# Kernel tuning notes

Hardware: AMD Instinct MI355X
Metric: run time of the kernel (lower is better)

The kernel has to match this reference:

```python
import jax, jax.numpy as jnp
import numpy as np

B, C, H, W = 512, 128, 7, 7
P = 21            # patch_size
DIL = 2           # dilation_patch
PAD = DIL * (P // 2)  # 20: max displacement in pixels


def setup_inputs() -> dict:
    key = jax.random.key(0)
    k1, k2, k3, k4 = jax.random.split(key, 4)
    patch1 = jax.random.normal(k1, (B, C, H, W), jnp.float32)
    patch2 = jax.random.normal(k2, (B, C, H, W), jnp.float32)
    feat = P * P * H * W  # 21609
    w_bbox = jax.random.normal(k3, (4, feat), jnp.float32) * (1.0 / np.sqrt(feat))
    b_bbox = jax.random.normal(k4, (4,), jnp.float32) * 0.01
    return {"patch1": patch1, "patch2": patch2, "w_bbox": w_bbox, "b_bbox": b_bbox}


def _correlation(patch1, patch2):
    """SpatialCorrelationSampler(patch_size=21, dilation_patch=2, kernel_size=1).

    out[b,p,q,i,j] = sum_c patch1[b,c,i,j] * patch2[b,c, i + 2*(p-10), j + 2*(q-10)]
    with zero padding for out-of-bounds displacements. Output: [B, 21, 21, 7, 7].
    """
    padded = jnp.pad(patch2, ((0, 0), (0, 0), (PAD, PAD), (PAD, PAD)))  # [B,C,47,47]
    # Outer product over spatial positions, contracted over channels:
    # T[b,i,j,u,v] = sum_c patch1[b,c,i,j] * padded[b,c,u,v]
    T = jnp.einsum('bcij,bcuv->bijuv', patch1, padded)  # [B,7,7,47,47]
    # Gather the displaced entries: u = 2p + i, v = 2q + j
    Pp, Qq, Ii, Jj = jnp.meshgrid(jnp.arange(P), jnp.arange(P),
                                  jnp.arange(H), jnp.arange(W), indexing='ij')
    corr = T[:, Ii, Jj, DIL * Pp + Ii, DIL * Qq + Jj]  # [B,21,21,7,7]
    return corr


def reference(patch1, patch2, w_bbox, b_bbox):
    corr = _correlation(patch1, patch2)           # [B,21,21,7,7]
    x = corr.reshape(corr.shape[0], -1)           # flatten(start_dim=1)
    return x @ w_bbox.T + b_bbox                  # [B,4]
```

## Files before the change

kernel.cpp:

```cpp
#include <hip/hip_runtime.h>

#define NB    512
#define FEAT  21609
#define CHW   6272
#define NV4   1568
#define PLANE 5120

__device__ __forceinline__ unsigned short f2bf(float x) {
    unsigned u = __float_as_uint(x);
    u += 0x7fffu + ((u >> 16) & 1u);
    return (unsigned short)(u >> 16);
}
__device__ __forceinline__ float bf2f(unsigned short h) {
    return __uint_as_float((unsigned)h << 16);
}

__global__ __launch_bounds__(256) void corr_head_kernel(
    const float* __restrict__ patch1,
    const float* __restrict__ patch2,
    const float* __restrict__ w_bbox,
    const float* __restrict__ b_bbox,
    float* __restrict__ out)
{
    __shared__ __align__(16) unsigned short s1b[CHW];
    __shared__ __align__(16) float          s2p[2 * PLANE];
    __shared__ __align__(16) ushort4        s_wq[784];
    __shared__ float s_red[16];

    const int tid = threadIdx.x;
    const int b   = blockIdx.x;

    for (int n = tid; n < 1024; n += 256) {
        int jp = n >> 9, c = (n >> 2) & 127, u = n & 3;
        s2p[jp * PLANE + c * 40 + 28 + u] = 0.f;
    }
    for (int n = tid; n < 896; n += 256) {
        int c = n / 7, i2 = n - 7 * c;
        s2p[PLANE + c * 40 + i2 * 4 + 3] = 0.f;
    }

    const float4* g1 = (const float4*)(patch1 + (size_t)b * CHW);
    for (int t = tid; t < NV4; t += 256) {
        float4 v = g1[t];
        ((ushort4*)s1b)[t] = make_ushort4(f2bf(v.x), f2bf(v.y), f2bf(v.z), f2bf(v.w));
    }

    const float4* g2 = (const float4*)(patch2 + (size_t)b * CHW);
    for (int t = tid; t < NV4; t += 256) {
        float4 v = g2[t];
        int e = t * 4;
        int c = e / 49;
        int r = e - 49 * c;
        #pragma unroll
        for (int k = 0; k < 4; ++k) {
            int i2 = (r * 37) >> 8;
            int j2 = r - 7 * i2;
            s2p[(j2 & 1) * PLANE + c * 40 + i2 * 4 + (j2 >> 1)] = (&v.x)[k];
            if (++r == 49) { r = 0; ++c; }
        }
    }

    for (int n = tid; n < 784; n += 256) {
        int ij = n % 49, tu = n / 49;
        int t = tu >> 2, u = tu & 3;
        int i = ij / 7, j = ij - 7 * i;
        int i2 = (i & 1) + 2 * t, j2 = (j & 1) + 2 * u;
        ushort4 wq = make_ushort4(0, 0, 0, 0);
        if (i2 < 7 && j2 < 7) {
            int p = 10 + ((i2 - i) >> 1);
            int q = 10 + ((j2 - j) >> 1);
            int f = ((p * 21 + q) * 7 + i) * 7 + j;
            wq = make_ushort4(f2bf(w_bbox[f]), f2bf(w_bbox[FEAT + f]),
                              f2bf(w_bbox[2 * FEAT + f]), f2bf(w_bbox[3 * FEAT + f]));
        }
        s_wq[n] = wq;
    }
    __syncthreads();

    float a0 = 0.f, a1 = 0.f, a2 = 0.f, a3 = 0.f;
    if (tid < 196) {
        const int ij = tid >> 2, cs = tid & 3;
        const int i = ij / 7, j = ij - 7 * i;
        const float* base2 = s2p + (j & 1) * PLANE + (i & 1) * 4;

        float dot[4][4];
        #pragma unroll
        for (int t = 0; t < 4; ++t)
            #pragma unroll
            for (int u = 0; u < 4; ++u) dot[t][u] = 0.f;

        #pragma unroll 2
        for (int cc = 0; cc < 32; ++cc) {
            int c = cs + 4 * cc;
            float f1 = bf2f(s1b[c * 49 + ij]);
            const float* bc = base2 + c * 40;
            #pragma unroll
            for (int t = 0; t < 4; ++t) {
                float4 f2 = *(const float4*)(bc + 8 * t);
                dot[t][0] = fmaf(f1, f2.x, dot[t][0]);
                dot[t][1] = fmaf(f1, f2.y, dot[t][1]);
                dot[t][2] = fmaf(f1, f2.z, dot[t][2]);
                dot[t][3] = fmaf(f1, f2.w, dot[t][3]);
            }
        }

        #pragma unroll
        for (int t = 0; t < 4; ++t)
            #pragma unroll
            for (int u = 0; u < 4; ++u) {
                ushort4 wq = s_wq[(4 * t + u) * 49 + ij];
                float d = dot[t][u];
                a0 = fmaf(d, bf2f(wq.x), a0);
                a1 = fmaf(d, bf2f(wq.y), a1);
                a2 = fmaf(d, bf2f(wq.z), a2);
                a3 = fmaf(d, bf2f(wq.w), a3);
            }
    }

    for (int off = 32; off > 0; off >>= 1) {
        a0 += __shfl_down(a0, off, 64);
        a1 += __shfl_down(a1, off, 64);
        a2 += __shfl_down(a2, off, 64);
        a3 += __shfl_down(a3, off, 64);
    }
    if ((tid & 63) == 0) {
        int w = tid >> 6;
        s_red[w * 4 + 0] = a0;
        s_red[w * 4 + 1] = a1;
        s_red[w * 4 + 2] = a2;
        s_red[w * 4 + 3] = a3;
    }
    __syncthreads();
    if (tid < 4) {
        float r = s_red[tid] + s_red[4 + tid] + s_red[8 + tid] + s_red[12 + tid];
        out[b * 4 + tid] = r + b_bbox[tid];
    }
}

extern "C" void kernel_launch(void* const* d_in, const int* in_sizes, int n_in,
                              void* d_out, int out_size, void* d_ws, size_t ws_size,
                              hipStream_t stream) {
    const float* patch1 = (const float*)d_in[0];
    const float* patch2 = (const float*)d_in[1];
    const float* w_bbox = (const float*)d_in[2];
    const float* b_bbox = (const float*)d_in[3];
    float* out = (float*)d_out;
    corr_head_kernel<<<dim3(NB), dim3(256), 0, stream>>>(patch1, patch2, w_bbox, b_bbox, out);
}
```

Baseline: 80.65 us.

## Prefetch all inputs into registers and overlap second half staging with compute

All global loads for patch1, patch2 and the weight gather are now issued up front into registers. The first half of the channels is written to shared memory and computed on while the second half and the weights are being staged. This is meant to hide global-load latency behind the first half's FMA work within each block. In exchange it uses more registers, which may lower occupancy, and adds an extra barrier.

```diff
diff --git a/kernel.cpp b/kernel.cpp
--- a/kernel.cpp
+++ b/kernel.cpp
@@ -3,8 +3,9 @@
 #define NB    512
 #define FEAT  21609
 #define CHW   6272
-#define NV4   1568
 #define PLANE 5120
+#define HV4   784
+#define HFLT  3136
 
 __device__ __forceinline__ unsigned short f2bf(float x) {
     unsigned u = __float_as_uint(x);
@@ -40,57 +41,75 @@
     }
 
     const float4* g1 = (const float4*)(patch1 + (size_t)b * CHW);
-    for (int t = tid; t < NV4; t += 256) {
-        float4 v = g1[t];
-        ((ushort4*)s1b)[t] = make_ushort4(f2bf(v.x), f2bf(v.y), f2bf(v.z), f2bf(v.w));
-    }
-
     const float4* g2 = (const float4*)(patch2 + (size_t)b * CHW);
-    for (int t = tid; t < NV4; t += 256) {
-        float4 v = g2[t];
-        int e = t * 4;
-        int c = e / 49;
-        int r = e - 49 * c;
+    float4 rp1[4], rp2[4], rq1[4], rq2[4];
+    #pragma unroll
+    for (int i = 0; i < 3; ++i) {
+        rp1[i] = g1[tid + 256 * i];
+        rp2[i] = g2[tid + 256 * i];
+        rq1[i] = g1[HV4 + tid + 256 * i];
+        rq2[i] = g2[HV4 + tid + 256 * i];
+    }
+    if (tid < 16) {
+        rp1[3] = g1[768 + tid];        rp2[3] = g2[768 + tid];
+        rq1[3] = g1[HV4 + 768 + tid];  rq2[3] = g2[HV4 + 768 + tid];
+    }
+
+    float wv[4][4];
+    #pragma unroll
+    for (int i = 0; i < 4; ++i) {
+        int n = tid + 256 * i;
+        wv[i][0] = wv[i][1] = wv[i][2] = wv[i][3] = 0.f;
+        if (n < 784) {
+            int ij = n % 49, tu = n / 49;
+            int t = tu >> 2, u = tu & 3;
+            int ii = ij / 7, jj = ij - 7 * ii;
+            int i2 = (ii & 1) + 2 * t, j2 = (jj & 1) + 2 * u;
+            if (i2 < 7 && j2 < 7) {
+                int p = 10 + ((i2 - ii) >> 1);
+                int q = 10 + ((j2 - jj) >> 1);
+                int f = ((p * 21 + q) * 7 + ii) * 7 + jj;
+                wv[i][0] = w_bbox[f];
+                wv[i][1] = w_bbox[FEAT + f];
+                wv[i][2] = w_bbox[2 * FEAT + f];
+                wv[i][3] = w_bbox[3 * FEAT + f];
+            }
+        }
+    }
+
+    #pragma unroll
+    for (int i = 0; i < 4; ++i) {
+        if (i < 3 || tid < 16) {
+            int t = tid + 256 * i;
+            float4 v = rp1[i];
+            ((ushort4*)s1b)[t] = make_ushort4(f2bf(v.x), f2bf(v.y), f2bf(v.z), f2bf(v.w));
+            float4 w = rp2[i];
+            int e = 4 * t;
+            int c = e / 49, r = e - 49 * c;
+            #pragma unroll
+            for (int k = 0; k < 4; ++k) {
+                int i2 = (r * 37) >> 8;
+                int j2 = r - 7 * i2;
+                s2p[(j2 & 1) * PLANE + c * 40 + i2 * 4 + (j2 >> 1)] = (&w.x)[k];
+                if (++r == 49) { r = 0; ++c; }
+            }
+        }
+    }
+    __syncthreads();
+
+    const int ij = tid >> 2, cs = tid & 3;
+    const int i = ij / 7, j = (tid < 196) ? (ij - 7 * i) : 0;
+    const float* base2 = s2p + (j & 1) * PLANE + (i & 1) * 4;
+
+    float dot[4][4];
+    #pragma unroll
+    for (int t = 0; t < 4; ++t)
         #pragma unroll
-        for (int k = 0; k < 4; ++k) {
-            int i2 = (r * 37) >> 8;
-            int j2 = r - 7 * i2;
-            s2p[(j2 & 1) * PLANE + c * 40 + i2 * 4 + (j2 >> 1)] = (&v.x)[k];
-            if (++r == 49) { r = 0; ++c; }
-        }
-    }
-
-    for (int n = tid; n < 784; n += 256) {
-        int ij = n % 49, tu = n / 49;
-        int t = tu >> 2, u = tu & 3;
-        int i = ij / 7, j = ij - 7 * i;
-        int i2 = (i & 1) + 2 * t, j2 = (j & 1) + 2 * u;
-        ushort4 wq = make_ushort4(0, 0, 0, 0);
-        if (i2 < 7 && j2 < 7) {
-            int p = 10 + ((i2 - i) >> 1);
-            int q = 10 + ((j2 - j) >> 1);
-            int f = ((p * 21 + q) * 7 + i) * 7 + j;
-            wq = make_ushort4(f2bf(w_bbox[f]), f2bf(w_bbox[FEAT + f]),
-                              f2bf(w_bbox[2 * FEAT + f]), f2bf(w_bbox[3 * FEAT + f]));
-        }
-        s_wq[n] = wq;
-    }
-    __syncthreads();
-
-    float a0 = 0.f, a1 = 0.f, a2 = 0.f, a3 = 0.f;
+        for (int u = 0; u < 4; ++u) dot[t][u] = 0.f;
+
     if (tid < 196) {
-        const int ij = tid >> 2, cs = tid & 3;
-        const int i = ij / 7, j = ij - 7 * i;
-        const float* base2 = s2p + (j & 1) * PLANE + (i & 1) * 4;
-
-        float dot[4][4];
-        #pragma unroll
-        for (int t = 0; t < 4; ++t)
-            #pragma unroll
-            for (int u = 0; u < 4; ++u) dot[t][u] = 0.f;
-
         #pragma unroll 2
-        for (int cc = 0; cc < 32; ++cc) {
+        for (int cc = 0; cc < 16; ++cc) {
             int c = cs + 4 * cc;
             float f1 = bf2f(s1b[c * 49 + ij]);
             const float* bc = base2 + c * 40;
@@ -103,7 +122,55 @@
                 dot[t][3] = fmaf(f1, f2.w, dot[t][3]);
             }
         }
-
+    }
+
+    #pragma unroll
+    for (int i4 = 0; i4 < 4; ++i4) {
+        if (i4 < 3 || tid < 16) {
+            int t = tid + 256 * i4;
+            float4 v = rq1[i4];
+            ((ushort4*)s1b)[HV4 + t] = make_ushort4(f2bf(v.x), f2bf(v.y), f2bf(v.z), f2bf(v.w));
+            float4 w = rq2[i4];
+            int e = HFLT + 4 * t;
+            int c = e / 49, r = e - 49 * c;
+            #pragma unroll
+            for (int k = 0; k < 4; ++k) {
+                int i2 = (r * 37) >> 8;
+                int j2 = r - 7 * i2;
+                s2p[(j2 & 1) * PLANE + c * 40 + i2 * 4 + (j2 >> 1)] = (&w.x)[k];
+                if (++r == 49) { r = 0; ++c; }
+            }
+        }
+    }
+
+    #pragma unroll
+    for (int i4 = 0; i4 < 4; ++i4) {
+        int n = tid + 256 * i4;
+        if (n < 784)
+            s_wq[n] = make_ushort4(f2bf(wv[i4][0]), f2bf(wv[i4][1]),
+                                   f2bf(wv[i4][2]), f2bf(wv[i4][3]));
+    }
+    __syncthreads();
+
+    if (tid < 196) {
+        #pragma unroll 2
+        for (int cc = 16; cc < 32; ++cc) {
+            int c = cs + 4 * cc;
+            float f1 = bf2f(s1b[c * 49 + ij]);
+            const float* bc = base2 + c * 40;
+            #pragma unroll
+            for (int t = 0; t < 4; ++t) {
+                float4 f2 = *(const float4*)(bc + 8 * t);
+                dot[t][0] = fmaf(f1, f2.x, dot[t][0]);
+                dot[t][1] = fmaf(f1, f2.y, dot[t][1]);
+                dot[t][2] = fmaf(f1, f2.z, dot[t][2]);
+                dot[t][3] = fmaf(f1, f2.w, dot[t][3]);
+            }
+        }
+    }
+
+    float a0 = 0.f, a1 = 0.f, a2 = 0.f, a3 = 0.f;
+    if (tid < 196) {
         #pragma unroll
         for (int t = 0; t < 4; ++t)
             #pragma unroll
```

New measurement: 82.03 us. About the same (+1.7%).

## Pair output positions sharing patch2 parity to reuse shared-memory loads

Applied to the files above, without the earlier changes.

Each thread now handles two spatial positions that share the same (i&1, j&1) parity class, chosen through constant lookup tables. The float4 reads of the patch2 plane are then reused for both positions. The channel split widens from 4 to 8 threads per slot, so 200 threads each do half as many channel iterations. This aims to cut LDS traffic per FMA, at the cost of more accumulator registers and an odd leftover slot that does redundant work.

```diff
diff --git a/kernel.cpp b/kernel.cpp
--- a/kernel.cpp
+++ b/kernel.cpp
@@ -5,6 +5,11 @@
 #define CHW   6272
 #define NV4   1568
 #define PLANE 5120
+
+__constant__ unsigned char c_pa[25] = {0,4,14,18,28,32,42,46,  1,5,17,29,33,45,
+                                       7,11,21,25,35,39,       8,12,24,36,40};
+__constant__ unsigned char c_pb[25] = {2,6,16,20,30,34,44,48,  3,15,19,31,43,47,
+                                       9,13,23,27,37,41,       10,22,26,38,255};
 
 __device__ __forceinline__ unsigned short f2bf(float x) {
     unsigned u = __float_as_uint(x);
@@ -78,29 +83,38 @@
     __syncthreads();
 
     float a0 = 0.f, a1 = 0.f, a2 = 0.f, a3 = 0.f;
-    if (tid < 196) {
-        const int ij = tid >> 2, cs = tid & 3;
-        const int i = ij / 7, j = ij - 7 * i;
+    if (tid < 200) {
+        const int slot = tid >> 3, cs = tid & 7;
+        const int ija  = c_pa[slot];
+        const int ijbr = c_pb[slot];
+        const bool has_b = (ijbr < 49);
+        const int ijb  = has_b ? ijbr : ija;
+        const int i = ija / 7, j = ija - 7 * i;
         const float* base2 = s2p + (j & 1) * PLANE + (i & 1) * 4;
 
-        float dot[4][4];
+        float da[4][4], db[4][4];
         #pragma unroll
         for (int t = 0; t < 4; ++t)
             #pragma unroll
-            for (int u = 0; u < 4; ++u) dot[t][u] = 0.f;
+            for (int u = 0; u < 4; ++u) { da[t][u] = 0.f; db[t][u] = 0.f; }
 
         #pragma unroll 2
-        for (int cc = 0; cc < 32; ++cc) {
-            int c = cs + 4 * cc;
-            float f1 = bf2f(s1b[c * 49 + ij]);
+        for (int cc = 0; cc < 16; ++cc) {
+            int c = cs + 8 * cc;
+            float f1a = bf2f(s1b[c * 49 + ija]);
+            float f1b = bf2f(s1b[c * 49 + ijb]);
             const float* bc = base2 + c * 40;
             #pragma unroll
             for (int t = 0; t < 4; ++t) {
                 float4 f2 = *(const float4*)(bc + 8 * t);
-                dot[t][0] = fmaf(f1, f2.x, dot[t][0]);
-                dot[t][1] = fmaf(f1, f2.y, dot[t][1]);
-                dot[t][2] = fmaf(f1, f2.z, dot[t][2]);
-                dot[t][3] = fmaf(f1, f2.w, dot[t][3]);
+                da[t][0] = fmaf(f1a, f2.x, da[t][0]);
+                da[t][1] = fmaf(f1a, f2.y, da[t][1]);
+                da[t][2] = fmaf(f1a, f2.z, da[t][2]);
+                da[t][3] = fmaf(f1a, f2.w, da[t][3]);
+                db[t][0] = fmaf(f1b, f2.x, db[t][0]);
+                db[t][1] = fmaf(f1b, f2.y, db[t][1]);
+                db[t][2] = fmaf(f1b, f2.z, db[t][2]);
+                db[t][3] = fmaf(f1b, f2.w, db[t][3]);
             }
         }
 
@@ -108,13 +122,26 @@
         for (int t = 0; t < 4; ++t)
             #pragma unroll
             for (int u = 0; u < 4; ++u) {
-                ushort4 wq = s_wq[(4 * t + u) * 49 + ij];
-                float d = dot[t][u];
+                ushort4 wq = s_wq[(4 * t + u) * 49 + ija];
+                float d = da[t][u];
                 a0 = fmaf(d, bf2f(wq.x), a0);
                 a1 = fmaf(d, bf2f(wq.y), a1);
                 a2 = fmaf(d, bf2f(wq.z), a2);
                 a3 = fmaf(d, bf2f(wq.w), a3);
             }
+        if (has_b) {
+            #pragma unroll
+            for (int t = 0; t < 4; ++t)
+                #pragma unroll
+                for (int u = 0; u < 4; ++u) {
+                    ushort4 wq = s_wq[(4 * t + u) * 49 + ijb];
+                    float d = db[t][u];
+                    a0 = fmaf(d, bf2f(wq.x), a0);
+                    a1 = fmaf(d, bf2f(wq.y), a1);
+                    a2 = fmaf(d, bf2f(wq.z), a2);
+                    a3 = fmaf(d, bf2f(wq.w), a3);
+                }
+        }
     }
 
     for (int off = 32; off > 0; off >>= 1) {
```

Measured after the change: 78.92 us. 2.1% less time.
